# Kernel tuning notes

Measured on AMD Instinct MI355X. Metric: run time of the kernel, lower is better.

## Reference

```python
import jax, jax.numpy as jnp
import numpy as np

S, B, I, H, O = 1024, 64, 512, 2048, 512


def setup_inputs() -> dict:
    key = jax.random.key(0)
    k1, k2, k3, k4, k5 = jax.random.split(key, 5)
    X = jax.random.normal(k1, (S, B, I), dtype=jnp.float32)
    W_ih = jax.random.normal(k2, (H, I), dtype=jnp.float32) * (1.0 / np.sqrt(I))
    hh = jax.random.uniform(k3, (H,), dtype=jnp.float32)  # clamped-to-[-1,1] diagonal recurrence
    W_ho = jax.random.normal(k4, (O, H), dtype=jnp.float32) * (1.0 / np.sqrt(H))
    b_ho = jax.random.normal(k5, (O,), dtype=jnp.float32) * 0.01
    return {"X": X, "W_ih": W_ih, "hh": hh, "W_ho": W_ho, "b_ho": b_ho}


def reference(X, W_ih, hh, W_ho, b_ho):
    # Batch the input->hidden projection over the whole sequence in one GEMM:
    # u[s,b,h] = X[s,b,i] @ W_ih[h,i]^T
    u = jnp.einsum('sbi,hi->sbh', X, W_ih)
    h0 = jnp.zeros((X.shape[1], W_ih.shape[0]), dtype=X.dtype)

    def step(h, u_t):
        h_new = jnp.abs(u_t + hh * h)
        return h_new, None

    h_final, _ = jax.lax.scan(step, h0, u)
    Y = h_final @ W_ho.T + b_ho  # [B, O]
    return Y
```

## Files before the change

kernel.cpp:

```cpp
#include <hip/hip_runtime.h>
#include <hip/hip_bf16.h>
#include <stdint.h>

#define S_LEN 1024
#define B_SZ  64
#define I_SZ  512
#define H_SZ  2048
#define O_SZ  512

typedef __bf16  bf16x8 __attribute__((ext_vector_type(8)));
typedef float   f32x4  __attribute__((ext_vector_type(4)));

static __device__ __forceinline__ ushort f2bf(float f) {
  union { float f; unsigned u; } v; v.f = f;
  unsigned r = v.u + 0x7FFFu + ((v.u >> 16) & 1u);
  return (ushort)(r >> 16);
}
static __device__ __forceinline__ float bf2f(ushort u) {
  return __builtin_bit_cast(float, (unsigned)u << 16);
}

#define GLOAD_LDS16(gp, lp) \
  __builtin_amdgcn_global_load_lds( \
      (__attribute__((address_space(1))) void*)(gp), \
      (__attribute__((address_space(3))) void*)(lp), 16, 0, 0)

__global__ __launch_bounds__(256) void convert_f32_bf16_kernel(
    const float4* __restrict__ in, ushort4* __restrict__ out, int n4) {
  int i = blockIdx.x * 256 + threadIdx.x;
  if (i >= n4) return;
  float4 v = in[i];
  ushort4 o; o.x = f2bf(v.x); o.y = f2bf(v.y); o.z = f2bf(v.z); o.w = f2bf(v.w);
  out[i] = o;
}

__global__ __launch_bounds__(256) void init_y_kernel(
    const float* __restrict__ bho, float* __restrict__ Y) {
  int idx = blockIdx.x * 256 + threadIdx.x;
  Y[idx] = bho[idx & (O_SZ - 1)];
}

#define CVT_WRITE_A() do { \
    _Pragma("unroll") \
    for (int j_ = 0; j_ < 4; ++j_) { \
      union { __bf16 h[8]; uint4 v; } uvt_; \
      uvt_.h[0] = (__bf16)ar[2*j_].x;   uvt_.h[1] = (__bf16)ar[2*j_].y; \
      uvt_.h[2] = (__bf16)ar[2*j_].z;   uvt_.h[3] = (__bf16)ar[2*j_].w; \
      uvt_.h[4] = (__bf16)ar[2*j_+1].x; uvt_.h[5] = (__bf16)ar[2*j_+1].y; \
      uvt_.h[6] = (__bf16)ar[2*j_+1].z; uvt_.h[7] = (__bf16)ar[2*j_+1].w; \
      *(uint4*)&As[(arow0 + j_ * 8) * 72 + (lane & 7) * 8] = uvt_.v; \
    } } while (0)

#define PREFETCH_A(T) do { \
    const float* gp_ = X + offA + (size_t)((T) >> 3) * (128 * B_SZ * I_SZ) \
                         + (size_t)(((T) & 7) * 64); \
    _Pragma("unroll") \
    for (int j_ = 0; j_ < 4; ++j_) { \
      ar[2*j_]   = *(const float4*)(gp_ + (size_t)j_ * (8 * B_SZ * I_SZ)); \
      ar[2*j_+1] = *(const float4*)(gp_ + (size_t)j_ * (8 * B_SZ * I_SZ) + 4); \
    } } while (0)

#define SCAN16(colp, s0_) do { \
    ushort4 v0 = *(const ushort4*)&(colp)[(s0_)]; \
    ushort4 v1 = *(const ushort4*)&(colp)[(s0_) + 4]; \
    ushort4 v2 = *(const ushort4*)&(colp)[(s0_) + 8]; \
    ushort4 v3 = *(const ushort4*)&(colp)[(s0_) + 12]; \
    p = fmaf(c, fabsf(p), bf2f(v0.x)); p = fmaf(c, fabsf(p), bf2f(v0.y)); \
    p = fmaf(c, fabsf(p), bf2f(v0.z)); p = fmaf(c, fabsf(p), bf2f(v0.w)); \
    p = fmaf(c, fabsf(p), bf2f(v1.x)); p = fmaf(c, fabsf(p), bf2f(v1.y)); \
    p = fmaf(c, fabsf(p), bf2f(v1.z)); p = fmaf(c, fabsf(p), bf2f(v1.w)); \
    p = fmaf(c, fabsf(p), bf2f(v2.x)); p = fmaf(c, fabsf(p), bf2f(v2.y)); \
    p = fmaf(c, fabsf(p), bf2f(v2.z)); p = fmaf(c, fabsf(p), bf2f(v2.w)); \
    p = fmaf(c, fabsf(p), bf2f(v3.x)); p = fmaf(c, fabsf(p), bf2f(v3.y)); \
    p = fmaf(c, fabsf(p), bf2f(v3.z)); p = fmaf(c, fabsf(p), bf2f(v3.w)); \
  } while (0)

__global__ __launch_bounds__(256, 2) void fused_gemm_scan_kernel(
    const float* __restrict__ X,
    const ushort* __restrict__ Wbf,
    const float* __restrict__ hh,
    const float* __restrict__ Who,
    float* __restrict__ Y) {
  __shared__ __align__(16) ushort smem[34304];
  ushort* As = smem;
  ushort* Bs = smem + 9216;
  ushort* Cs = smem + 17408;

  const int tid  = threadIdx.x;
  const int wave = tid >> 6;
  const int lane = tid & 63;

  const int bid = blockIdx.x;
  const int xcd = bid & 7;
  const int g   = bid >> 3;
  const int b   = (xcd << 3) | (g & 7);
  const int ht  = g >> 3;

  const int wm = (wave >> 1) * 64;
  const int wn = (wave & 1) * 64;
  const int ml = lane & 15;
  const int q  = lane >> 4;

  const int arow0 = wave * 32 + (lane >> 3);
  const size_t offA = (size_t)arow0 * (B_SZ * I_SZ) + (size_t)b * I_SZ
                    + (size_t)((lane & 7) * 8);

  const int r0     = wave * 32;
  const int srow   = lane >> 3;
  const int schunk = ((lane & 7) - srow) & 7;
  const ushort* gB = Wbf + (size_t)(ht * 128 + r0 + srow) * I_SZ + schunk * 8;
  ushort* lB = Bs + r0 * 64;

  const int aoff0 = q * 8;
  const int aoff1 = (4 + q) * 8;
  const int boff0 = ((q + ml) & 7) * 8;
  const int boff1 = ((4 + q + ml) & 7) * 8;
  int arow[4], brow[4];
  #pragma unroll
  for (int i = 0; i < 4; ++i) {
    arow[i] = (wm + i * 16 + ml) * 72;
    brow[i] = (wn + i * 16 + ml) * 64;
  }

  float c = 0.0f, p = 0.0f;
  if (tid < 128) c = hh[ht * 128 + tid];

  float4 ar[8];

  #pragma unroll
  for (int jj = 0; jj < 4; ++jj)
    GLOAD_LDS16(gB + (size_t)(jj * 8) * I_SZ, lB + jj * 512);
  __builtin_amdgcn_sched_barrier(0);
  PREFETCH_A(0);
  CVT_WRITE_A();
  PREFETCH_A(1);
  __builtin_amdgcn_sched_barrier(0);
  asm volatile("s_waitcnt vmcnt(8) lgkmcnt(0)" ::: "memory");
  __builtin_amdgcn_sched_barrier(0);
  __builtin_amdgcn_s_barrier();

  f32x4 acc[4][4];

  #pragma unroll 1
  for (int t = 0; t < 64; ++t) {
    const int kt = t & 7;
    if (kt == 0) {
      #pragma unroll
      for (int mi = 0; mi < 4; ++mi)
        #pragma unroll
        for (int ni = 0; ni < 4; ++ni) {
          f32x4 z = {0.f, 0.f, 0.f, 0.f};
          acc[mi][ni] = z;
        }
    }

    bf16x8 a0[4], a1[4], b0[4], b1[4];
    #pragma unroll
    for (int i = 0; i < 4; ++i) {
      a0[i] = *(const bf16x8*)&As[arow[i] + aoff0];
      a1[i] = *(const bf16x8*)&As[arow[i] + aoff1];
      b0[i] = *(const bf16x8*)&Bs[brow[i] + boff0];
      b1[i] = *(const bf16x8*)&Bs[brow[i] + boff1];
    }
    __builtin_amdgcn_sched_barrier(0);
    asm volatile("s_waitcnt lgkmcnt(0)" ::: "memory");
    __builtin_amdgcn_sched_barrier(0);
    __builtin_amdgcn_s_barrier();

    if (t < 63) {
      const int k1 = (t + 1) & 7;
      #pragma unroll
      for (int jj = 0; jj < 4; ++jj)
        GLOAD_LDS16(gB + (size_t)(jj * 8) * I_SZ + k1 * 64, lB + jj * 512);
    }
    __builtin_amdgcn_sched_barrier(0);
    if (t < 63) {
      CVT_WRITE_A();
      if (t < 62) PREFETCH_A(t + 2);
    }

    if (t >= 8 && tid < 128) {
      const ushort* col = &Cs[tid * 132];
      const int s0 = kt * 16;
      SCAN16(col, s0);
    }

    __builtin_amdgcn_s_setprio(1);
    #pragma unroll
    for (int mi = 0; mi < 4; ++mi)
      #pragma unroll
      for (int ni = 0; ni < 4; ++ni)
        acc[mi][ni] = __builtin_amdgcn_mfma_f32_16x16x32_bf16(
            a0[mi], b0[ni], acc[mi][ni], 0, 0, 0);
    #pragma unroll
    for (int mi = 0; mi < 4; ++mi)
      #pragma unroll
      for (int ni = 0; ni < 4; ++ni)
        acc[mi][ni] = __builtin_amdgcn_mfma_f32_16x16x32_bf16(
            a1[mi], b1[ni], acc[mi][ni], 0, 0, 0);
    __builtin_amdgcn_s_setprio(0);

    __builtin_amdgcn_sched_barrier(0);
    if (t < 62) {
      asm volatile("s_waitcnt vmcnt(8) lgkmcnt(0)" ::: "memory");
    } else {
      asm volatile("s_waitcnt vmcnt(0) lgkmcnt(0)" ::: "memory");
    }
    __builtin_amdgcn_sched_barrier(0);
    __builtin_amdgcn_s_barrier();

    if (kt == 7) {
      const int sb = wm + q * 4;
      #pragma unroll
      for (int mi = 0; mi < 4; ++mi)
        #pragma unroll
        for (int ni = 0; ni < 4; ++ni) {
          ushort4 o;
          o.x = f2bf(acc[mi][ni][0]); o.y = f2bf(acc[mi][ni][1]);
          o.z = f2bf(acc[mi][ni][2]); o.w = f2bf(acc[mi][ni][3]);
          *(ushort4*)&Cs[(wn + ni * 16 + ml) * 132 + sb + mi * 16] = o;
        }
    }
  }

  __syncthreads();

  if (tid < 128) {
    const ushort* col = &Cs[tid * 132];
    #pragma unroll
    for (int s0 = 0; s0 < 128; s0 += 16) {
      SCAN16(col, s0);
    }
    ((float*)smem)[tid] = fabsf(p);
  }
  __syncthreads();

  {
    const float* hs = (const float*)smem;
    const float* w0 = Who + (size_t)tid * H_SZ + (size_t)ht * 128;
    const float* w1 = w0 + (size_t)256 * H_SZ;
    float y0 = 0.f, y1 = 0.f;
    #pragma unroll 8
    for (int k = 0; k < 128; k += 4) {
      float4 hv = *(const float4*)&hs[k];
      float4 u0 = *(const float4*)&w0[k];
      float4 u1 = *(const float4*)&w1[k];
      y0 += hv.x * u0.x + hv.y * u0.y + hv.z * u0.z + hv.w * u0.w;
      y1 += hv.x * u1.x + hv.y * u1.y + hv.z * u1.z + hv.w * u1.w;
    }
    atomicAdd(&Y[(size_t)b * O_SZ + tid], y0);
    atomicAdd(&Y[(size_t)b * O_SZ + 256 + tid], y1);
  }
}

extern "C" void kernel_launch(void* const* d_in, const int* in_sizes, int n_in,
                              void* d_out, int out_size, void* d_ws, size_t ws_size,
                              hipStream_t stream) {
  (void)in_sizes; (void)n_in; (void)out_size; (void)ws_size;
  const float* X   = (const float*)d_in[0];
  const float* Wih = (const float*)d_in[1];
  const float* hh  = (const float*)d_in[2];
  const float* Who = (const float*)d_in[3];
  const float* bho = (const float*)d_in[4];
  float* Y = (float*)d_out;

  ushort* Wbf = (ushort*)d_ws;

  {
    int n4w = (int)((size_t)H_SZ * I_SZ / 4);
    convert_f32_bf16_kernel<<<n4w / 256, 256, 0, stream>>>(
        (const float4*)Wih, (ushort4*)Wbf, n4w);
  }

  init_y_kernel<<<(B_SZ * O_SZ) / 256, 256, 0, stream>>>(bho, Y);

  fused_gemm_scan_kernel<<<1024, 256, 0, stream>>>(X, Wbf, hh, Who, Y);
}
```

Before: 418.1 us.

## Double-buffer A prefetch registers and split MFMA k-loop into halves

Restructures the main GEMM/scan loop into a macro body unrolled by two. The body ping-pongs between two register buffers for the fp32 X prefetch and issues that prefetch at the start of each step. Each tile's K dimension is processed in two halves, loading only the fragments for the current half before its MFMAs, which lowers register pressure. The hand-placed s_waitcnt vmcnt/sched_barrier sequences are replaced with plain __syncthreads. The barriers may force outstanding global loads to drain every step, which would lose the prior partial-wait overlap.

```diff
diff --git a/kernel.cpp b/kernel.cpp
--- a/kernel.cpp
+++ b/kernel.cpp
@@ -40,24 +40,24 @@
   Y[idx] = bho[idx & (O_SZ - 1)];
 }
 
-#define CVT_WRITE_A() do { \
-    _Pragma("unroll") \
-    for (int j_ = 0; j_ < 4; ++j_) { \
-      union { __bf16 h[8]; uint4 v; } uvt_; \
-      uvt_.h[0] = (__bf16)ar[2*j_].x;   uvt_.h[1] = (__bf16)ar[2*j_].y; \
-      uvt_.h[2] = (__bf16)ar[2*j_].z;   uvt_.h[3] = (__bf16)ar[2*j_].w; \
-      uvt_.h[4] = (__bf16)ar[2*j_+1].x; uvt_.h[5] = (__bf16)ar[2*j_+1].y; \
-      uvt_.h[6] = (__bf16)ar[2*j_+1].z; uvt_.h[7] = (__bf16)ar[2*j_+1].w; \
-      *(uint4*)&As[(arow0 + j_ * 8) * 72 + (lane & 7) * 8] = uvt_.v; \
-    } } while (0)
-
-#define PREFETCH_A(T) do { \
+#define PREF(AR, T) do { \
     const float* gp_ = X + offA + (size_t)((T) >> 3) * (128 * B_SZ * I_SZ) \
                          + (size_t)(((T) & 7) * 64); \
     _Pragma("unroll") \
     for (int j_ = 0; j_ < 4; ++j_) { \
-      ar[2*j_]   = *(const float4*)(gp_ + (size_t)j_ * (8 * B_SZ * I_SZ)); \
-      ar[2*j_+1] = *(const float4*)(gp_ + (size_t)j_ * (8 * B_SZ * I_SZ) + 4); \
+      AR[2*j_]   = *(const float4*)(gp_ + (size_t)j_ * (8 * B_SZ * I_SZ)); \
+      AR[2*j_+1] = *(const float4*)(gp_ + (size_t)j_ * (8 * B_SZ * I_SZ) + 4); \
+    } } while (0)
+
+#define CVTW(AR) do { \
+    _Pragma("unroll") \
+    for (int j_ = 0; j_ < 4; ++j_) { \
+      union { __bf16 h[8]; uint4 v; } uvt_; \
+      uvt_.h[0] = (__bf16)AR[2*j_].x;   uvt_.h[1] = (__bf16)AR[2*j_].y; \
+      uvt_.h[2] = (__bf16)AR[2*j_].z;   uvt_.h[3] = (__bf16)AR[2*j_].w; \
+      uvt_.h[4] = (__bf16)AR[2*j_+1].x; uvt_.h[5] = (__bf16)AR[2*j_+1].y; \
+      uvt_.h[6] = (__bf16)AR[2*j_+1].z; uvt_.h[7] = (__bf16)AR[2*j_+1].w; \
+      *(uint4*)&As[(arow0 + j_ * 8) * 72 + (lane & 7) * 8] = uvt_.v; \
     } } while (0)
 
 #define SCAN16(colp, s0_) do { \
@@ -75,6 +75,63 @@
     p = fmaf(c, fabsf(p), bf2f(v3.z)); p = fmaf(c, fabsf(p), bf2f(v3.w)); \
   } while (0)
 
+#define BODY(T, CUR, NXT) do { \
+    const int t_ = (T); \
+    const int kt_ = t_ & 7; \
+    if (kt_ == 0) { \
+      _Pragma("unroll") \
+      for (int mi_ = 0; mi_ < 4; ++mi_) \
+        _Pragma("unroll") \
+        for (int ni_ = 0; ni_ < 4; ++ni_) { \
+          f32x4 z_ = {0.f, 0.f, 0.f, 0.f}; \
+          acc[mi_][ni_] = z_; \
+        } \
+    } \
+    if (t_ < 62) { PREF(NXT, t_ + 2); } \
+    _Pragma("unroll") \
+    for (int ks_ = 0; ks_ < 2; ++ks_) { \
+      bf16x8 af_[4], bf_[4]; \
+      _Pragma("unroll") \
+      for (int i_ = 0; i_ < 4; ++i_) { \
+        af_[i_] = *(const bf16x8*)&As[arow[i_] + (ks_ * 4 + q) * 8]; \
+        bf_[i_] = *(const bf16x8*)&Bs[brow[i_] + boff[ks_]]; \
+      } \
+      __builtin_amdgcn_s_setprio(1); \
+      _Pragma("unroll") \
+      for (int mi_ = 0; mi_ < 4; ++mi_) \
+        _Pragma("unroll") \
+        for (int ni_ = 0; ni_ < 4; ++ni_) \
+          acc[mi_][ni_] = __builtin_amdgcn_mfma_f32_16x16x32_bf16( \
+              af_[mi_], bf_[ni_], acc[mi_][ni_], 0, 0, 0); \
+      __builtin_amdgcn_s_setprio(0); \
+    } \
+    __syncthreads();   \
+    if (t_ < 63) { \
+      const int k1_ = (t_ + 1) & 7; \
+      _Pragma("unroll") \
+      for (int jj_ = 0; jj_ < 4; ++jj_) \
+        GLOAD_LDS16(gB + (size_t)(jj_ * 8) * I_SZ + k1_ * 64, lB + jj_ * 512); \
+      CVTW(CUR); \
+    } \
+    if (t_ >= 8 && tid < 128) { \
+      const ushort* col_ = &Cs[tid * 132]; \
+      SCAN16(col_, kt_ * 16); \
+    } \
+    __syncthreads();   \
+    if (kt_ == 7) { \
+      const int sb_ = wm + q * 4; \
+      _Pragma("unroll") \
+      for (int mi_ = 0; mi_ < 4; ++mi_) \
+        _Pragma("unroll") \
+        for (int ni_ = 0; ni_ < 4; ++ni_) { \
+          ushort4 o_; \
+          o_.x = f2bf(acc[mi_][ni_][0]); o_.y = f2bf(acc[mi_][ni_][1]); \
+          o_.z = f2bf(acc[mi_][ni_][2]); o_.w = f2bf(acc[mi_][ni_][3]); \
+          *(ushort4*)&Cs[(wn + ni_ * 16 + ml) * 132 + sb_ + mi_ * 16] = o_; \
+        } \
+    } \
+  } while (0)
+
 __global__ __launch_bounds__(256, 2) void fused_gemm_scan_kernel(
     const float* __restrict__ X,
     const ushort* __restrict__ Wbf,
@@ -111,10 +168,9 @@
   const ushort* gB = Wbf + (size_t)(ht * 128 + r0 + srow) * I_SZ + schunk * 8;
   ushort* lB = Bs + r0 * 64;
 
-  const int aoff0 = q * 8;
-  const int aoff1 = (4 + q) * 8;
-  const int boff0 = ((q + ml) & 7) * 8;
-  const int boff1 = ((4 + q + ml) & 7) * 8;
+  int boff[2];
+  boff[0] = ((q + ml) & 7) * 8;
+  boff[1] = ((4 + q + ml) & 7) * 8;
   int arow[4], brow[4];
   #pragma unroll
   for (int i = 0; i < 4; ++i) {
@@ -125,102 +181,21 @@
   float c = 0.0f, p = 0.0f;
   if (tid < 128) c = hh[ht * 128 + tid];
 
-  float4 ar[8];
-
+  float4 arA[8], arB[8];
+  f32x4 acc[4][4];
+
+  PREF(arA, 0);
   #pragma unroll
   for (int jj = 0; jj < 4; ++jj)
     GLOAD_LDS16(gB + (size_t)(jj * 8) * I_SZ, lB + jj * 512);
-  __builtin_amdgcn_sched_barrier(0);
-  PREFETCH_A(0);
-  CVT_WRITE_A();
-  PREFETCH_A(1);
-  __builtin_amdgcn_sched_barrier(0);
-  asm volatile("s_waitcnt vmcnt(8) lgkmcnt(0)" ::: "memory");
-  __builtin_amdgcn_sched_barrier(0);
-  __builtin_amdgcn_s_barrier();
-
-  f32x4 acc[4][4];
+  CVTW(arA);
+  PREF(arA, 1);
+  __syncthreads();
 
   #pragma unroll 1
-  for (int t = 0; t < 64; ++t) {
-    const int kt = t & 7;
-    if (kt == 0) {
-      #pragma unroll
-      for (int mi = 0; mi < 4; ++mi)
-        #pragma unroll
-        for (int ni = 0; ni < 4; ++ni) {
-          f32x4 z = {0.f, 0.f, 0.f, 0.f};
-          acc[mi][ni] = z;
-        }
-    }
-
-    bf16x8 a0[4], a1[4], b0[4], b1[4];
-    #pragma unroll
-    for (int i = 0; i < 4; ++i) {
-      a0[i] = *(const bf16x8*)&As[arow[i] + aoff0];
-      a1[i] = *(const bf16x8*)&As[arow[i] + aoff1];
-      b0[i] = *(const bf16x8*)&Bs[brow[i] + boff0];
-      b1[i] = *(const bf16x8*)&Bs[brow[i] + boff1];
-    }
-    __builtin_amdgcn_sched_barrier(0);
-    asm volatile("s_waitcnt lgkmcnt(0)" ::: "memory");
-    __builtin_amdgcn_sched_barrier(0);
-    __builtin_amdgcn_s_barrier();
-
-    if (t < 63) {
-      const int k1 = (t + 1) & 7;
-      #pragma unroll
-      for (int jj = 0; jj < 4; ++jj)
-        GLOAD_LDS16(gB + (size_t)(jj * 8) * I_SZ + k1 * 64, lB + jj * 512);
-    }
-    __builtin_amdgcn_sched_barrier(0);
-    if (t < 63) {
-      CVT_WRITE_A();
-      if (t < 62) PREFETCH_A(t + 2);
-    }
-
-    if (t >= 8 && tid < 128) {
-      const ushort* col = &Cs[tid * 132];
-      const int s0 = kt * 16;
-      SCAN16(col, s0);
-    }
-
-    __builtin_amdgcn_s_setprio(1);
-    #pragma unroll
-    for (int mi = 0; mi < 4; ++mi)
-      #pragma unroll
-      for (int ni = 0; ni < 4; ++ni)
-        acc[mi][ni] = __builtin_amdgcn_mfma_f32_16x16x32_bf16(
-            a0[mi], b0[ni], acc[mi][ni], 0, 0, 0);
-    #pragma unroll
-    for (int mi = 0; mi < 4; ++mi)
-      #pragma unroll
-      for (int ni = 0; ni < 4; ++ni)
-        acc[mi][ni] = __builtin_amdgcn_mfma_f32_16x16x32_bf16(
-            a1[mi], b1[ni], acc[mi][ni], 0, 0, 0);
-    __builtin_amdgcn_s_setprio(0);
-
-    __builtin_amdgcn_sched_barrier(0);
-    if (t < 62) {
-      asm volatile("s_waitcnt vmcnt(8) lgkmcnt(0)" ::: "memory");
-    } else {
-      asm volatile("s_waitcnt vmcnt(0) lgkmcnt(0)" ::: "memory");
-    }
-    __builtin_amdgcn_sched_barrier(0);
-    __builtin_amdgcn_s_barrier();
-
-    if (kt == 7) {
-      const int sb = wm + q * 4;
-      #pragma unroll
-      for (int mi = 0; mi < 4; ++mi)
-        #pragma unroll
-        for (int ni = 0; ni < 4; ++ni) {
-          ushort4 o;
-          o.x = f2bf(acc[mi][ni][0]); o.y = f2bf(acc[mi][ni][1]);
-          o.z = f2bf(acc[mi][ni][2]); o.w = f2bf(acc[mi][ni][3]);
-          *(ushort4*)&Cs[(wn + ni * 16 + ml) * 132 + sb + mi * 16] = o;
-        }
-    }
+  for (int tt = 0; tt < 32; ++tt) {
+    BODY(2 * tt,     arA, arB);
+    BODY(2 * tt + 1, arB, arA);
   }
 
   __syncthreads();
```

Measured after the change: 406.6 us. -2.8%, faster.

## Pre-convert X to transposed bf16 and simplify fused GEMM-scan pipeline

Applied to the files above, without the earlier changes.

Adds a separate kernel that converts X to bf16 in batch-major layout, so the fused kernel can load A tiles straight into LDS with global_load_lds, as it already does for B, instead of doing register float loads and conversion. The fused kernel drops its hand-pipelined prefetch and waitcnt schedule in favour of a simple sync-load-sync loop per k-tile. It shares LDS between the A tile and the C buffer to shrink shared memory and allows 3 blocks per CU. The cost is an extra full pass over X, a 128MB read and 64MB write, plus a scan that is no longer overlapped with MFMA and loads that are no longer double-buffered.

```diff
diff --git a/kernel.cpp b/kernel.cpp
--- a/kernel.cpp
+++ b/kernel.cpp
@@ -34,31 +34,25 @@
   out[i] = o;
 }
 
+__global__ __launch_bounds__(256) void convert_x_kernel(
+    const float* __restrict__ X, ushort* __restrict__ Xt) {
+  const int row  = blockIdx.x * 4 + (threadIdx.x >> 6);
+  const int lane = threadIdx.x & 63;
+  const int s = row >> 6, b = row & 63;
+  const float* src = X + (size_t)row * I_SZ + lane * 8;
+  float4 v0 = *(const float4*)src;
+  float4 v1 = *(const float4*)(src + 4);
+  union { ushort h[8]; uint4 v; } o;
+  o.h[0] = f2bf(v0.x); o.h[1] = f2bf(v0.y); o.h[2] = f2bf(v0.z); o.h[3] = f2bf(v0.w);
+  o.h[4] = f2bf(v1.x); o.h[5] = f2bf(v1.y); o.h[6] = f2bf(v1.z); o.h[7] = f2bf(v1.w);
+  *(uint4*)(Xt + ((size_t)b * S_LEN + s) * I_SZ + lane * 8) = o.v;
+}
+
 __global__ __launch_bounds__(256) void init_y_kernel(
     const float* __restrict__ bho, float* __restrict__ Y) {
   int idx = blockIdx.x * 256 + threadIdx.x;
   Y[idx] = bho[idx & (O_SZ - 1)];
 }
-
-#define CVT_WRITE_A() do { \
-    _Pragma("unroll") \
-    for (int j_ = 0; j_ < 4; ++j_) { \
-      union { __bf16 h[8]; uint4 v; } uvt_; \
-      uvt_.h[0] = (__bf16)ar[2*j_].x;   uvt_.h[1] = (__bf16)ar[2*j_].y; \
-      uvt_.h[2] = (__bf16)ar[2*j_].z;   uvt_.h[3] = (__bf16)ar[2*j_].w; \
-      uvt_.h[4] = (__bf16)ar[2*j_+1].x; uvt_.h[5] = (__bf16)ar[2*j_+1].y; \
-      uvt_.h[6] = (__bf16)ar[2*j_+1].z; uvt_.h[7] = (__bf16)ar[2*j_+1].w; \
-      *(uint4*)&As[(arow0 + j_ * 8) * 72 + (lane & 7) * 8] = uvt_.v; \
-    } } while (0)
-
-#define PREFETCH_A(T) do { \
-    const float* gp_ = X + offA + (size_t)((T) >> 3) * (128 * B_SZ * I_SZ) \
-                         + (size_t)(((T) & 7) * 64); \
-    _Pragma("unroll") \
-    for (int j_ = 0; j_ < 4; ++j_) { \
-      ar[2*j_]   = *(const float4*)(gp_ + (size_t)j_ * (8 * B_SZ * I_SZ)); \
-      ar[2*j_+1] = *(const float4*)(gp_ + (size_t)j_ * (8 * B_SZ * I_SZ) + 4); \
-    } } while (0)
 
 #define SCAN16(colp, s0_) do { \
     ushort4 v0 = *(const ushort4*)&(colp)[(s0_)]; \
@@ -75,16 +69,16 @@
     p = fmaf(c, fabsf(p), bf2f(v3.z)); p = fmaf(c, fabsf(p), bf2f(v3.w)); \
   } while (0)
 
-__global__ __launch_bounds__(256, 2) void fused_gemm_scan_kernel(
-    const float* __restrict__ X,
+__global__ __launch_bounds__(256, 3) void fused_gemm_scan_kernel(
+    const ushort* __restrict__ Xbf,
     const ushort* __restrict__ Wbf,
     const float* __restrict__ hh,
     const float* __restrict__ Who,
     float* __restrict__ Y) {
-  __shared__ __align__(16) ushort smem[34304];
+  __shared__ __align__(16) ushort smem[16896];
   ushort* As = smem;
-  ushort* Bs = smem + 9216;
-  ushort* Cs = smem + 17408;
+  ushort* Bs = smem + 8192;
+  ushort* Cs = smem;
 
   const int tid  = threadIdx.x;
   const int wave = tid >> 6;
@@ -101,138 +95,86 @@
   const int ml = lane & 15;
   const int q  = lane >> 4;
 
-  const int arow0 = wave * 32 + (lane >> 3);
-  const size_t offA = (size_t)arow0 * (B_SZ * I_SZ) + (size_t)b * I_SZ
-                    + (size_t)((lane & 7) * 8);
-
   const int r0     = wave * 32;
   const int srow   = lane >> 3;
   const int schunk = ((lane & 7) - srow) & 7;
+  const ushort* gA = Xbf + (size_t)b * (S_LEN * I_SZ)
+                   + (size_t)(r0 + srow) * I_SZ + schunk * 8;
   const ushort* gB = Wbf + (size_t)(ht * 128 + r0 + srow) * I_SZ + schunk * 8;
+  ushort* lA = As + r0 * 64;
   ushort* lB = Bs + r0 * 64;
 
-  const int aoff0 = q * 8;
-  const int aoff1 = (4 + q) * 8;
-  const int boff0 = ((q + ml) & 7) * 8;
-  const int boff1 = ((4 + q + ml) & 7) * 8;
+  int foff[2];
+  foff[0] = ((q + ml) & 7) * 8;
+  foff[1] = ((4 + q + ml) & 7) * 8;
   int arow[4], brow[4];
   #pragma unroll
   for (int i = 0; i < 4; ++i) {
-    arow[i] = (wm + i * 16 + ml) * 72;
+    arow[i] = (wm + i * 16 + ml) * 64;
     brow[i] = (wn + i * 16 + ml) * 64;
   }
 
   float c = 0.0f, p = 0.0f;
   if (tid < 128) c = hh[ht * 128 + tid];
 
-  float4 ar[8];
-
-  #pragma unroll
-  for (int jj = 0; jj < 4; ++jj)
-    GLOAD_LDS16(gB + (size_t)(jj * 8) * I_SZ, lB + jj * 512);
-  __builtin_amdgcn_sched_barrier(0);
-  PREFETCH_A(0);
-  CVT_WRITE_A();
-  PREFETCH_A(1);
-  __builtin_amdgcn_sched_barrier(0);
-  asm volatile("s_waitcnt vmcnt(8) lgkmcnt(0)" ::: "memory");
-  __builtin_amdgcn_sched_barrier(0);
-  __builtin_amdgcn_s_barrier();
-
-  f32x4 acc[4][4];
-
   #pragma unroll 1
-  for (int t = 0; t < 64; ++t) {
-    const int kt = t & 7;
-    if (kt == 0) {
-      #pragma unroll
-      for (int mi = 0; mi < 4; ++mi)
+  for (int st = 0; st < 8; ++st) {
+    f32x4 acc[4][4] = {};
+
+    for (int kt = 0; kt < 8; ++kt) {
+      __syncthreads();
+      const ushort* ga = gA + (size_t)st * (128 * I_SZ) + kt * 64;
+      const ushort* gb = gB + kt * 64;
+      #pragma unroll
+      for (int jj = 0; jj < 4; ++jj) {
+        GLOAD_LDS16(ga + (size_t)(jj * 8) * I_SZ, lA + jj * 512);
+        GLOAD_LDS16(gb + (size_t)(jj * 8) * I_SZ, lB + jj * 512);
+      }
+      __syncthreads();
+      #pragma unroll
+      for (int ks = 0; ks < 2; ++ks) {
+        bf16x8 af[4], bfr[4];
         #pragma unroll
-        for (int ni = 0; ni < 4; ++ni) {
-          f32x4 z = {0.f, 0.f, 0.f, 0.f};
-          acc[mi][ni] = z;
+        for (int i = 0; i < 4; ++i) {
+          af[i]  = *(const bf16x8*)&As[arow[i] + foff[ks]];
+          bfr[i] = *(const bf16x8*)&Bs[brow[i] + foff[ks]];
         }
-    }
-
-    bf16x8 a0[4], a1[4], b0[4], b1[4];
+        __builtin_amdgcn_s_setprio(1);
+        #pragma unroll
+        for (int mi = 0; mi < 4; ++mi)
+          #pragma unroll
+          for (int ni = 0; ni < 4; ++ni)
+            acc[mi][ni] = __builtin_amdgcn_mfma_f32_16x16x32_bf16(
+                af[mi], bfr[ni], acc[mi][ni], 0, 0, 0);
+        __builtin_amdgcn_s_setprio(0);
+      }
+    }
+
+    __syncthreads();
+    const int sb = wm + q * 4;
     #pragma unroll
-    for (int i = 0; i < 4; ++i) {
-      a0[i] = *(const bf16x8*)&As[arow[i] + aoff0];
-      a1[i] = *(const bf16x8*)&As[arow[i] + aoff1];
-      b0[i] = *(const bf16x8*)&Bs[brow[i] + boff0];
-      b1[i] = *(const bf16x8*)&Bs[brow[i] + boff1];
-    }
-    __builtin_amdgcn_sched_barrier(0);
-    asm volatile("s_waitcnt lgkmcnt(0)" ::: "memory");
-    __builtin_amdgcn_sched_barrier(0);
-    __builtin_amdgcn_s_barrier();
-
-    if (t < 63) {
-      const int k1 = (t + 1) & 7;
-      #pragma unroll
-      for (int jj = 0; jj < 4; ++jj)
-        GLOAD_LDS16(gB + (size_t)(jj * 8) * I_SZ + k1 * 64, lB + jj * 512);
-    }
-    __builtin_amdgcn_sched_barrier(0);
-    if (t < 63) {
-      CVT_WRITE_A();
-      if (t < 62) PREFETCH_A(t + 2);
-    }
-
-    if (t >= 8 && tid < 128) {
+    for (int mi = 0; mi < 4; ++mi) {
+      #pragma unroll
+      for (int ni = 0; ni < 4; ++ni) {
+        ushort4 o;
+        o.x = f2bf(acc[mi][ni][0]); o.y = f2bf(acc[mi][ni][1]);
+        o.z = f2bf(acc[mi][ni][2]); o.w = f2bf(acc[mi][ni][3]);
+        *(ushort4*)&Cs[(wn + ni * 16 + ml) * 132 + sb + mi * 16] = o;
+      }
+    }
+    __syncthreads();
+
+    if (tid < 128) {
       const ushort* col = &Cs[tid * 132];
-      const int s0 = kt * 16;
-      SCAN16(col, s0);
-    }
-
-    __builtin_amdgcn_s_setprio(1);
-    #pragma unroll
-    for (int mi = 0; mi < 4; ++mi)
-      #pragma unroll
-      for (int ni = 0; ni < 4; ++ni)
-        acc[mi][ni] = __builtin_amdgcn_mfma_f32_16x16x32_bf16(
-            a0[mi], b0[ni], acc[mi][ni], 0, 0, 0);
-    #pragma unroll
-    for (int mi = 0; mi < 4; ++mi)
-      #pragma unroll
-      for (int ni = 0; ni < 4; ++ni)
-        acc[mi][ni] = __builtin_amdgcn_mfma_f32_16x16x32_bf16(
-            a1[mi], b1[ni], acc[mi][ni], 0, 0, 0);
-    __builtin_amdgcn_s_setprio(0);
-
-    __builtin_amdgcn_sched_barrier(0);
-    if (t < 62) {
-      asm volatile("s_waitcnt vmcnt(8) lgkmcnt(0)" ::: "memory");
-    } else {
-      asm volatile("s_waitcnt vmcnt(0) lgkmcnt(0)" ::: "memory");
-    }
-    __builtin_amdgcn_sched_barrier(0);
-    __builtin_amdgcn_s_barrier();
-
-    if (kt == 7) {
-      const int sb = wm + q * 4;
-      #pragma unroll
-      for (int mi = 0; mi < 4; ++mi)
-        #pragma unroll
-        for (int ni = 0; ni < 4; ++ni) {
-          ushort4 o;
-          o.x = f2bf(acc[mi][ni][0]); o.y = f2bf(acc[mi][ni][1]);
-          o.z = f2bf(acc[mi][ni][2]); o.w = f2bf(acc[mi][ni][3]);
-          *(ushort4*)&Cs[(wn + ni * 16 + ml) * 132 + sb + mi * 16] = o;
-        }
+      #pragma unroll
+      for (int s0 = 0; s0 < 128; s0 += 16) {
+        SCAN16(col, s0);
+      }
     }
   }
 
   __syncthreads();
-
-  if (tid < 128) {
-    const ushort* col = &Cs[tid * 132];
-    #pragma unroll
-    for (int s0 = 0; s0 < 128; s0 += 16) {
-      SCAN16(col, s0);
-    }
-    ((float*)smem)[tid] = fabsf(p);
-  }
+  if (tid < 128) ((float*)smem)[tid] = fabsf(p);
   __syncthreads();
 
   {
@@ -264,7 +206,10 @@
   const float* bho = (const float*)d_in[4];
   float* Y = (float*)d_out;
 
-  ushort* Wbf = (ushort*)d_ws;
+  const size_t WBF = (size_t)H_SZ * I_SZ * 2;
+  char* w = (char*)d_ws;
+  ushort* Wbf = (ushort*)w;
+  ushort* Xbf = (ushort*)(w + WBF);
 
   {
     int n4w = (int)((size_t)H_SZ * I_SZ / 4);
@@ -272,7 +217,9 @@
         (const float4*)Wih, (ushort4*)Wbf, n4w);
   }
 
+  convert_x_kernel<<<(S_LEN * B_SZ) / 4, 256, 0, stream>>>(X, Xbf);
+
   init_y_kernel<<<(B_SZ * O_SZ) / 256, 256, 0, stream>>>(bho, Y);
 
-  fused_gemm_scan_kernel<<<1024, 256, 0, stream>>>(X, Wbf, hh, Who, Y);
-}
+  fused_gemm_scan_kernel<<<1024, 256, 0, stream>>>(Xbf, Wbf, hh, Who, Y);
+}
```

Result: no change. 413.3 us (-1.2%).
